# Performance work log

Hardware: AMD Instinct MI355X
Metric: run time of the kernel (lower is better)

## Reference

```python
import jax, jax.numpy as jnp
import numpy as np

BN_EPS = 1e-5

def _conv1x1(w, b, x):
    # w: (O, C), b: (O,), x: (B, C, T) -> (B, O, T)
    return jnp.einsum('oc,bct->bot', w, x) + b[None, :, None]

def _maxpool2(x):
    # MaxPool1d(kernel_size=2, stride=2): (B, C, T) -> (B, C, T//2)
    B, C, T = x.shape
    return x.reshape(B, C, T // 2, 2).max(axis=-1)

def setup_inputs() -> dict:
    key = jax.random.key(0)
    ks = jax.random.split(key, 11)
    B, C, Ci, T = 4, 256, 128, 8192
    s_in = 1.0 / np.sqrt(C)
    s_ic = 1.0 / np.sqrt(Ci)
    return {
        'x':       jax.random.normal(ks[0], (B, C, T), dtype=jnp.float32),
        'theta_w': jax.random.uniform(ks[1], (Ci, C), jnp.float32, -s_in, s_in),
        'theta_b': jax.random.uniform(ks[2], (Ci,),   jnp.float32, -s_in, s_in),
        'phi_w':   jax.random.uniform(ks[3], (Ci, C), jnp.float32, -s_in, s_in),
        'phi_b':   jax.random.uniform(ks[4], (Ci,),   jnp.float32, -s_in, s_in),
        'g_w':     jax.random.uniform(ks[5], (Ci, C), jnp.float32, -s_in, s_in),
        'g_b':     jax.random.uniform(ks[6], (Ci,),   jnp.float32, -s_in, s_in),
        'w_w':     jax.random.uniform(ks[7], (C, Ci), jnp.float32, -s_ic, s_ic),
        'w_b':     jax.random.uniform(ks[8], (C,),    jnp.float32, -s_ic, s_ic),
        'gamma':   jax.random.normal(ks[9], (C,), dtype=jnp.float32),
        'beta':    jax.random.normal(ks[10], (C,), dtype=jnp.float32),
    }

def reference(x, theta_w, theta_b, phi_w, phi_b, g_w, g_b, w_w, w_b, gamma, beta):
    # x: (B, C, T)
    theta = _conv1x1(theta_w, theta_b, x)            # (B, Ci, T)
    phi   = _maxpool2(_conv1x1(phi_w, phi_b, x))     # (B, Ci, N), N = T//2
    g     = _maxpool2(_conv1x1(g_w, g_b, x))         # (B, Ci, N)
    N = phi.shape[-1]
    # f = theta^T phi / N  (dot-product similarity, divide-by-N normalization)
    f = jnp.einsum('bct,bcn->btn', theta, phi) / N   # (B, T, N)
    y = jnp.einsum('btn,bcn->bct', f, g)             # (B, Ci, T)
    wy = _conv1x1(w_w, w_b, y)                       # (B, C, T)
    # BatchNorm1d (training mode: batch statistics over (B, T), biased var)
    mean = wy.mean(axis=(0, 2), keepdims=True)
    var = ((wy - mean) ** 2).mean(axis=(0, 2), keepdims=True)
    bn = gamma[None, :, None] * (wy - mean) * jax.lax.rsqrt(var + BN_EPS) + beta[None, :, None]
    return bn + x
```

## Files before the change

### kernel.cpp

```cpp
#include <hip/hip_runtime.h>
#include <hip/hip_bf16.h>


constexpr int B = 4, C = 256, CI = 128, T = 8192, NN = 4096;

using s16x8 = __attribute__((ext_vector_type(8))) short;
using f32x4 = __attribute__((ext_vector_type(4))) float;

__device__ __forceinline__ unsigned short f2bf(float f) {
    unsigned int x = __float_as_uint(f);
    unsigned int r = (x + 0x7fffu + ((x >> 16) & 1u)) >> 16;
    return (unsigned short)r;
}
__device__ __forceinline__ float bf2f(unsigned short u) {
    return __uint_as_float((unsigned int)u << 16);
}

#define MFMA(a, b, c) __builtin_amdgcn_mfma_f32_16x16x32_bf16((a), (b), (c), 0, 0, 0)

__device__ __forceinline__ void glds16(const unsigned short* g, void* l) {
    __builtin_amdgcn_global_load_lds(
        (const __attribute__((address_space(1))) unsigned int*)(g),
        (__attribute__((address_space(3))) unsigned int*)(l), 16, 0, 0);
}


constexpr size_t SZ_XT = (size_t)B * T * C * 2;
constexpr size_t O_XTH = 0;
constexpr size_t O_XTL = O_XTH + SZ_XT;
constexpr size_t O_WSH = O_XTL + SZ_XT;
constexpr size_t O_WSL = O_WSH + (size_t)C * C * 2;
constexpr size_t SZ_P  = (size_t)B * CI * NN * 2;
constexpr size_t O_PH  = O_WSL + (size_t)C * C * 2;
constexpr size_t O_PL  = O_PH + SZ_P;
constexpr size_t O_GH  = O_PL + SZ_P;
constexpr size_t O_GL  = O_GH + SZ_P;
constexpr size_t O_S   = O_GL + SZ_P;
constexpr size_t O_M   = O_S  + (size_t)B * CI * CI * 4;
constexpr size_t O_W2H = O_M  + (size_t)B * C * CI * 4;
constexpr size_t O_W2L = O_W2H + (size_t)B * C * C * 2;
constexpr size_t O_B2  = O_W2L + (size_t)B * C * C * 2;
constexpr size_t O_GS  = O_B2 + (size_t)B * C * 4;
constexpr size_t O_GQ  = O_GS + (size_t)C * 4;
constexpr size_t O_A   = O_GQ + (size_t)C * 4;
constexpr size_t O_SH  = O_A  + (size_t)C * 4;

__global__ __launch_bounds__(256) void k0_split(
    const float* __restrict__ x, unsigned short* __restrict__ xth,
    unsigned short* __restrict__ xtl)
{
    __shared__ float xs[64][65];
    int t0 = blockIdx.x * 64, c0 = blockIdx.y * 64, b = blockIdx.z;
    int tid = threadIdx.x;
    const float* xb = x + (size_t)b * C * T;
    #pragma unroll
    for (int p = 0; p < 4; ++p) {
        int idx = tid + p * 256;
        int cr = idx >> 4;
        int tg = (idx & 15) * 4;
        float4 v = *reinterpret_cast<const float4*>(xb + (size_t)(c0 + cr) * T + t0 + tg);
        xs[tg + 0][cr] = v.x; xs[tg + 1][cr] = v.y;
        xs[tg + 2][cr] = v.z; xs[tg + 3][cr] = v.w;
    }
    __syncthreads();
    size_t tileBase = ((size_t)b * (T / 128) + (t0 >> 7)) * 32768;
    int trBase = t0 & 127;
    #pragma unroll
    for (int p = 0; p < 2; ++p) {
        int idx = tid + p * 256;
        int kcL = idx >> 6;
        int tl  = idx & 63;
        s16x8 hs, ls;
        #pragma unroll
        for (int j = 0; j < 8; ++j) {
            float v = xs[tl][kcL * 8 + j];
            unsigned short h = f2bf(v);
            unsigned short l = f2bf(v - bf2f(h));
            hs[j] = (short)h; ls[j] = (short)l;
        }
        size_t dst = tileBase + (size_t)((c0 >> 3) + kcL) * 1024 + (trBase + tl) * 8;
        *reinterpret_cast<s16x8*>(xth + dst) = hs;
        *reinterpret_cast<s16x8*>(xtl + dst) = ls;
    }
}

__global__ __launch_bounds__(256) void k0w(
    const float* __restrict__ phi_w, const float* __restrict__ g_w,
    unsigned short* __restrict__ wsh, unsigned short* __restrict__ wsl)
{
    int idx = blockIdx.x * 256 + threadIdx.x;
    int c8 = idx & 31, row = idx >> 5;
    const float* src = (row < CI) ? &phi_w[(size_t)row * C + c8 * 8]
                                  : &g_w[(size_t)(row - CI) * C + c8 * 8];
    s16x8 hs, ls;
    #pragma unroll
    for (int j = 0; j < 8; ++j) {
        float v = src[j];
        unsigned short h = f2bf(v);
        hs[j] = (short)h; ls[j] = (short)f2bf(v - bf2f(h));
    }
    size_t dst = (size_t)(row >> 7) * 32768 + (size_t)c8 * 1024 + (row & 127) * 8;
    *reinterpret_cast<s16x8*>(wsh + dst) = hs;
    *reinterpret_cast<s16x8*>(wsl + dst) = ls;
}

#define STAGE_A(srcT) {                                                        \
    _Pragma("unroll")                                                          \
    for (int i_ = 0; i_ < 16; ++i_)                                            \
        glds16((srcT) + (size_t)(w * 8192 + i_ * 512 + lane * 8),              \
               arena + w * 16384 + i_ * 1024);                                 \
}

#define K8(BT) {                                                               \
    _Pragma("unroll")                                                          \
    for (int ks_ = 0; ks_ < 8; ++ks_) {                                        \
        s16x8 af[4], bfr[4];                                                   \
        _Pragma("unroll")                                                      \
        for (int ts_ = 0; ts_ < 4; ++ts_)                                      \
            af[ts_] = *(const s16x8*)(arena + (ks_ * 4 + lk) * 2048            \
                                      + (wt * 64 + ts_ * 16 + lr) * 16);       \
        _Pragma("unroll")                                                      \
        for (int os_ = 0; os_ < 4; ++os_)                                      \
            bfr[os_] = *(const s16x8*)((BT) + (size_t)(ks_ * 4 + lk) * 1024    \
                                       + (wo * 64 + os_ * 16 + lr) * 8);       \
        _Pragma("unroll")                                                      \
        for (int os_ = 0; os_ < 4; ++os_)                                      \
            _Pragma("unroll")                                                  \
            for (int ts_ = 0; ts_ < 4; ++ts_)                                  \
                acc[os_][ts_] = MFMA(af[ts_], bfr[os_], acc[os_][ts_]);        \
    }                                                                          \
}

#define GEMM_3PHASE(aT_h, aT_l, bT_h, bT_l) {                                  \
    STAGE_A(aT_h);                                                             \
    __syncthreads();                                                           \
    K8(bT_h);                                                                  \
    K8(bT_l);                                                                  \
    __syncthreads();                                                           \
    STAGE_A(aT_l);                                                             \
    __syncthreads();                                                           \
    K8(bT_h);                                                                  \
}

__global__ __launch_bounds__(256) void k1_mfma(
    const unsigned short* __restrict__ xth, const unsigned short* __restrict__ xtl,
    const unsigned short* __restrict__ wsh, const unsigned short* __restrict__ wsl,
    const float* __restrict__ phi_b, const float* __restrict__ g_b,
    unsigned short* __restrict__ ph, unsigned short* __restrict__ pl,
    unsigned short* __restrict__ gh, unsigned short* __restrict__ gl)
{
    const int b = blockIdx.z, t0 = blockIdx.x * 128, isG = blockIdx.y;
    __shared__ __align__(16) char arena[65536];
    const int tid = threadIdx.x, lane = tid & 63, w = tid >> 6;
    const int lr = lane & 15, lk = lane >> 4;
    const int wt = w >> 1, wo = w & 1;

    const unsigned short* aTh = xth + ((size_t)b * (T / 128) + (t0 >> 7)) * 32768;
    const unsigned short* aTl = xtl + ((size_t)b * (T / 128) + (t0 >> 7)) * 32768;
    const unsigned short* bTh = wsh + (size_t)isG * 32768;
    const unsigned short* bTl = wsl + (size_t)isG * 32768;

    f32x4 acc[4][4];
    #pragma unroll
    for (int i = 0; i < 4; ++i)
        #pragma unroll
        for (int j = 0; j < 4; ++j) acc[i][j] = (f32x4){0.f, 0.f, 0.f, 0.f};

    GEMM_3PHASE(aTh, aTl, bTh, bTl)
    __syncthreads();

    unsigned int (*pool_s)[65] = (unsigned int (*)[65])arena;
    const float* biasArr = isG ? g_b : phi_b;
    #pragma unroll
    for (int os = 0; os < 4; ++os) {
        int oL = wo * 64 + os * 16 + lr;
        float bias = biasArr[oL];
        #pragma unroll
        for (int ts = 0; ts < 4; ++ts) {
            f32x4 v = acc[os][ts];
            float m0 = fmaxf(v[0], v[1]) + bias;
            float m1 = fmaxf(v[2], v[3]) + bias;
            int nl = wt * 32 + ts * 8 + lk * 2;
            unsigned short h0 = f2bf(m0), h1 = f2bf(m1);
            pool_s[oL][nl]     = (unsigned int)h0 | ((unsigned int)f2bf(m0 - bf2f(h0)) << 16);
            pool_s[oL][nl + 1] = (unsigned int)h1 | ((unsigned int)f2bf(m1 - bf2f(h1)) << 16);
        }
    }
    __syncthreads();
    int oL = tid >> 1, seg = tid & 1;
    size_t n0 = (size_t)(t0 >> 1) + seg * 32;
    unsigned short* dh = (isG ? gh : ph) + ((size_t)b * CI + oL) * NN + n0;
    unsigned short* dl = (isG ? gl : pl) + ((size_t)b * CI + oL) * NN + n0;
    #pragma unroll
    for (int g4 = 0; g4 < 4; ++g4) {
        s16x8 hs, ls;
        #pragma unroll
        for (int j = 0; j < 8; ++j) {
            unsigned int u = pool_s[oL][seg * 32 + g4 * 8 + j];
            hs[j] = (short)(u & 0xffffu);
            ls[j] = (short)(u >> 16);
        }
        *reinterpret_cast<s16x8*>(dh + g4 * 8) = hs;
        *reinterpret_cast<s16x8*>(dl + g4 * 8) = ls;
    }
}

template <int MODE>
__global__ __launch_bounds__(256) void k45_mfma(
    const unsigned short* __restrict__ xth, const unsigned short* __restrict__ xtl,
    const unsigned short* __restrict__ w2h, const unsigned short* __restrict__ w2l,
    const float* __restrict__ b2, const float* __restrict__ x,
    const float* __restrict__ abuf, const float* __restrict__ shbuf,
    float* __restrict__ gsum, float* __restrict__ gsq, float* __restrict__ out)
{
    const int b = blockIdx.z, t0 = blockIdx.x * 128, oHalf = blockIdx.y;
    const int o0 = oHalf * 128;
    __shared__ __align__(16) char arena[65536];
    const int tid = threadIdx.x, lane = tid & 63, w = tid >> 6;
    const int lr = lane & 15, lk = lane >> 4;
    const int wt = w >> 1, wo = w & 1;

    const unsigned short* aTh = xth + ((size_t)b * (T / 128) + (t0 >> 7)) * 32768;
    const unsigned short* aTl = xtl + ((size_t)b * (T / 128) + (t0 >> 7)) * 32768;
    const unsigned short* bTh = w2h + ((size_t)b * 2 + oHalf) * 32768;
    const unsigned short* bTl = w2l + ((size_t)b * 2 + oHalf) * 32768;

    f32x4 acc[4][4];
    #pragma unroll
    for (int i = 0; i < 4; ++i)
        #pragma unroll
        for (int j = 0; j < 4; ++j) acc[i][j] = (f32x4){0.f, 0.f, 0.f, 0.f};

    GEMM_3PHASE(aTh, aTl, bTh, bTl)

    #pragma unroll
    for (int os = 0; os < 4; ++os) {
        int o = o0 + wo * 64 + os * 16 + lr;
        float bv = b2[(size_t)b * C + o];
        if (MODE == 0) {
            float s = 0.f, q = 0.f;
            #pragma unroll
            for (int ts = 0; ts < 4; ++ts)
                #pragma unroll
                for (int r = 0; r < 4; ++r) {
                    float v = acc[os][ts][r] + bv;
                    s += v; q += v * v;
                }
            s += __shfl_xor(s, 16); s += __shfl_xor(s, 32);
            q += __shfl_xor(q, 16); q += __shfl_xor(q, 32);
            if (lk == 0) { atomicAdd(&gsum[o], s); atomicAdd(&gsq[o], q); }
        } else {
            float av = abuf[o], sv = shbuf[o];
            #pragma unroll
            for (int ts = 0; ts < 4; ++ts) {
                int t = t0 + wt * 64 + ts * 16 + lk * 4;
                size_t base = ((size_t)b * C + o) * T + t;
                float4 xv = *reinterpret_cast<const float4*>(x + base);
                float4 ov;
                ov.x = av * (acc[os][ts][0] + bv) + sv + xv.x;
                ov.y = av * (acc[os][ts][1] + bv) + sv + xv.y;
                ov.z = av * (acc[os][ts][2] + bv) + sv + xv.z;
                ov.w = av * (acc[os][ts][3] + bv) + sv + xv.w;
                *reinterpret_cast<float4*>(out + base) = ov;
            }
        }
    }
}

__global__ __launch_bounds__(256) void k2_mfma(
    const unsigned short* __restrict__ ph, const unsigned short* __restrict__ pl,
    const unsigned short* __restrict__ gh, const unsigned short* __restrict__ gl,
    float* __restrict__ S)
{
    int b = blockIdx.y, n0 = blockIdx.x * 128;
    int tid = threadIdx.x, lane = tid & 63, w = tid >> 6;
    int lr = lane & 15, lk = lane >> 4;

    f32x4 acc[2][8];
    #pragma unroll
    for (int i = 0; i < 2; ++i)
        #pragma unroll
        for (int j = 0; j < 8; ++j) acc[i][j] = (f32x4){0.f, 0.f, 0.f, 0.f};

    const unsigned short* ah_b = gh + ((size_t)b * CI + w * 32 + lr) * NN + n0 + lk * 8;
    const unsigned short* al_b = gl + ((size_t)b * CI + w * 32 + lr) * NN + n0 + lk * 8;
    const unsigned short* bh_b = ph + ((size_t)b * CI + lr) * NN + n0 + lk * 8;
    const unsigned short* bl_b = pl + ((size_t)b * CI + lr) * NN + n0 + lk * 8;

    for (int ks = 0; ks < 4; ++ks) {
        s16x8 Ah[2], Al[2], Bh[8], Bl[8];
        #pragma unroll
        for (int is = 0; is < 2; ++is) {
            Ah[is] = *reinterpret_cast<const s16x8*>(ah_b + (size_t)is * 16 * NN + ks * 32);
            Al[is] = *reinterpret_cast<const s16x8*>(al_b + (size_t)is * 16 * NN + ks * 32);
        }
        #pragma unroll
        for (int js = 0; js < 8; ++js) {
            Bh[js] = *reinterpret_cast<const s16x8*>(bh_b + (size_t)js * 16 * NN + ks * 32);
            Bl[js] = *reinterpret_cast<const s16x8*>(bl_b + (size_t)js * 16 * NN + ks * 32);
        }
        #pragma unroll
        for (int is = 0; is < 2; ++is)
            #pragma unroll
            for (int js = 0; js < 8; ++js) {
                acc[is][js] = MFMA(Ah[is], Bh[js], acc[is][js]);
                acc[is][js] = MFMA(Al[is], Bh[js], acc[is][js]);
                acc[is][js] = MFMA(Ah[is], Bl[js], acc[is][js]);
            }
    }
    #pragma unroll
    for (int is = 0; is < 2; ++is) {
        int i0 = w * 32 + is * 16 + lk * 4;
        #pragma unroll
        for (int js = 0; js < 8; ++js) {
            int j = js * 16 + lr;
            #pragma unroll
            for (int r = 0; r < 4; ++r)
                atomicAdd(&S[((size_t)b * CI + i0 + r) * CI + j], acc[is][js][r]);
        }
    }
}

__global__ __launch_bounds__(256) void k3a_M(
    const float* __restrict__ w_w, const float* __restrict__ S, float* __restrict__ M)
{
    int idx = blockIdx.x * 256 + threadIdx.x;
    int j4 = (idx & 31) * 4;
    int r  = (idx >> 5) & (C - 1);
    int b  = idx >> 13;
    const float* Sb = S + (size_t)b * CI * CI;
    const float* wr = w_w + (size_t)r * CI;
    float4 a = {0.f, 0.f, 0.f, 0.f};
    for (int k = 0; k < CI; ++k) {
        float wv = wr[k];
        float4 s = *reinterpret_cast<const float4*>(&Sb[(size_t)k * CI + j4]);
        a.x += wv * s.x; a.y += wv * s.y; a.z += wv * s.z; a.w += wv * s.w;
    }
    const float sc = 1.f / NN;
    a.x *= sc; a.y *= sc; a.z *= sc; a.w *= sc;
    *reinterpret_cast<float4*>(&M[((size_t)b * C + r) * CI + j4]) = a;
}

__global__ __launch_bounds__(256) void k3b_W2(
    const float* __restrict__ M, const float* __restrict__ theta_w,
    const float* __restrict__ theta_b, const float* __restrict__ w_b,
    unsigned short* __restrict__ w2h, unsigned short* __restrict__ w2l,
    float* __restrict__ b2)
{
    int idx = blockIdx.x * 256 + threadIdx.x;
    int c8 = idx & 31;
    int r  = (idx >> 5) & (C - 1);
    int b  = idx >> 13;
    const float* Mb = M + ((size_t)b * C + r) * CI;
    float4 a0 = {0.f, 0.f, 0.f, 0.f}, a1 = {0.f, 0.f, 0.f, 0.f};
    for (int k = 0; k < CI; ++k) {
        float mv = Mb[k];
        const float* tw = &theta_w[(size_t)k * C + c8 * 8];
        float4 t0 = *reinterpret_cast<const float4*>(tw);
        float4 t1 = *reinterpret_cast<const float4*>(tw + 4);
        a0.x += mv * t0.x; a0.y += mv * t0.y; a0.z += mv * t0.z; a0.w += mv * t0.w;
        a1.x += mv * t1.x; a1.y += mv * t1.y; a1.z += mv * t1.z; a1.w += mv * t1.w;
    }
    float av[8] = {a0.x, a0.y, a0.z, a0.w, a1.x, a1.y, a1.z, a1.w};
    s16x8 hs, ls;
    #pragma unroll
    for (int i = 0; i < 8; ++i) {
        unsigned short h = f2bf(av[i]);
        hs[i] = (short)h; ls[i] = (short)f2bf(av[i] - bf2f(h));
    }
    size_t dst = ((size_t)b * 2 + (r >> 7)) * 32768 + (size_t)c8 * 1024 + (r & 127) * 8;
    *reinterpret_cast<s16x8*>(w2h + dst) = hs;
    *reinterpret_cast<s16x8*>(w2l + dst) = ls;
    if (c8 == 0) {
        float bv = 0.f;
        for (int k = 0; k < CI; ++k) bv += Mb[k] * theta_b[k];
        b2[(size_t)b * C + r] = bv + w_b[r];
    }
}

__global__ void k4b_stats(const float* __restrict__ gsum, const float* __restrict__ gsq,
                          const float* __restrict__ gamma, const float* __restrict__ beta,
                          float* __restrict__ a, float* __restrict__ sh)
{
    int c = threadIdx.x;
    const float invBT = 1.f / (float)(B * T);
    float mean = gsum[c] * invBT;
    float var  = gsq[c] * invBT - mean * mean;
    float av = gamma[c] * rsqrtf(var + 1e-5f);
    a[c]  = av;
    sh[c] = beta[c] - av * mean;
}

extern "C" void kernel_launch(void* const* d_in, const int* in_sizes, int n_in,
                              void* d_out, int out_size, void* d_ws, size_t ws_size,
                              hipStream_t stream)
{
    const float* x       = (const float*)d_in[0];
    const float* theta_w = (const float*)d_in[1];
    const float* theta_b = (const float*)d_in[2];
    const float* phi_w   = (const float*)d_in[3];
    const float* phi_b   = (const float*)d_in[4];
    const float* g_w     = (const float*)d_in[5];
    const float* g_b     = (const float*)d_in[6];
    const float* w_w     = (const float*)d_in[7];
    const float* w_b     = (const float*)d_in[8];
    const float* gamma   = (const float*)d_in[9];
    const float* beta    = (const float*)d_in[10];
    float* out = (float*)d_out;
    char* ws = (char*)d_ws;

    unsigned short* xth = (unsigned short*)(ws + O_XTH);
    unsigned short* xtl = (unsigned short*)(ws + O_XTL);
    unsigned short* wsh = (unsigned short*)(ws + O_WSH);
    unsigned short* wsl = (unsigned short*)(ws + O_WSL);
    unsigned short* ph  = (unsigned short*)(ws + O_PH);
    unsigned short* pl  = (unsigned short*)(ws + O_PL);
    unsigned short* gh  = (unsigned short*)(ws + O_GH);
    unsigned short* gl  = (unsigned short*)(ws + O_GL);
    float* Sbuf  = (float*)(ws + O_S);
    float* Mbuf  = (float*)(ws + O_M);
    unsigned short* w2h = (unsigned short*)(ws + O_W2H);
    unsigned short* w2l = (unsigned short*)(ws + O_W2L);
    float* b2    = (float*)(ws + O_B2);
    float* gsum  = (float*)(ws + O_GS);
    float* gsq   = (float*)(ws + O_GQ);
    float* abuf  = (float*)(ws + O_A);
    float* shbuf = (float*)(ws + O_SH);

    hipMemsetAsync(Sbuf, 0, (size_t)B * CI * CI * sizeof(float), stream);
    hipMemsetAsync(gsum, 0, 2 * (size_t)C * sizeof(float), stream);

    k0_split<<<dim3(T / 64, C / 64, B), 256, 0, stream>>>(x, xth, xtl);
    k0w<<<dim3(32), 256, 0, stream>>>(phi_w, g_w, wsh, wsl);
    k1_mfma<<<dim3(T / 128, 2, B), 256, 0, stream>>>(xth, xtl, wsh, wsl, phi_b, g_b,
                                                     ph, pl, gh, gl);
    k2_mfma<<<dim3(NN / 128, B), 256, 0, stream>>>(ph, pl, gh, gl, Sbuf);
    k3a_M<<<dim3(B * C * CI / 4 / 256), 256, 0, stream>>>(w_w, Sbuf, Mbuf);
    k3b_W2<<<dim3(B * C * C / 8 / 256), 256, 0, stream>>>(Mbuf, theta_w, theta_b, w_b,
                                                          w2h, w2l, b2);
    k45_mfma<0><<<dim3(T / 128, C / 128, B), 256, 0, stream>>>(
        xth, xtl, w2h, w2l, b2, x, abuf, shbuf, gsum, gsq, out);
    k4b_stats<<<1, C, 0, stream>>>(gsum, gsq, gamma, beta, abuf, shbuf);
    k45_mfma<1><<<dim3(T / 128, C / 128, B), 256, 0, stream>>>(
        xth, xtl, w2h, w2l, b2, x, abuf, shbuf, gsum, gsq, out);
}
```

Measured before the change: 253.4 us.

## Store bf16 conv output once and apply BatchNorm in a streaming pass

The first output GEMM pass now writes the pre-BN result as bf16 into scratch memory that reuses the phi buffer, while also accumulating the per-channel statistics. A new elementwise kernel then applies the BN scale, shift and residual, replacing the second full GEMM recomputation. Several MFMA kernels also get launch bounds requesting two blocks per CU. Rounding wy to bf16 reduces output precision and adds an extra write and read of the intermediate.

```diff
diff --git a/kernel.cpp b/kernel.cpp
--- a/kernel.cpp
+++ b/kernel.cpp
@@ -35,6 +35,7 @@
 constexpr size_t O_PL  = O_PH + SZ_P;
 constexpr size_t O_GH  = O_PL + SZ_P;
 constexpr size_t O_GL  = O_GH + SZ_P;
+constexpr size_t O_WY  = O_PH;
 constexpr size_t O_S   = O_GL + SZ_P;
 constexpr size_t O_M   = O_S  + (size_t)B * CI * CI * 4;
 constexpr size_t O_W2H = O_M  + (size_t)B * C * CI * 4;
@@ -142,7 +143,7 @@
     K8(bT_h);                                                                  \
 }
 
-__global__ __launch_bounds__(256) void k1_mfma(
+__global__ __launch_bounds__(256, 2) void k1_mfma(
     const unsigned short* __restrict__ xth, const unsigned short* __restrict__ xtl,
     const unsigned short* __restrict__ wsh, const unsigned short* __restrict__ wsl,
     const float* __restrict__ phi_b, const float* __restrict__ g_b,
@@ -205,13 +206,11 @@
     }
 }
 
-template <int MODE>
-__global__ __launch_bounds__(256) void k45_mfma(
+__global__ __launch_bounds__(256, 2) void k45_stats(
     const unsigned short* __restrict__ xth, const unsigned short* __restrict__ xtl,
     const unsigned short* __restrict__ w2h, const unsigned short* __restrict__ w2l,
-    const float* __restrict__ b2, const float* __restrict__ x,
-    const float* __restrict__ abuf, const float* __restrict__ shbuf,
-    float* __restrict__ gsum, float* __restrict__ gsq, float* __restrict__ out)
+    const float* __restrict__ b2, unsigned short* __restrict__ wy,
+    float* __restrict__ gsum, float* __restrict__ gsq)
 {
     const int b = blockIdx.z, t0 = blockIdx.x * 128, oHalf = blockIdx.y;
     const int o0 = oHalf * 128;
@@ -237,37 +236,62 @@
     for (int os = 0; os < 4; ++os) {
         int o = o0 + wo * 64 + os * 16 + lr;
         float bv = b2[(size_t)b * C + o];
-        if (MODE == 0) {
-            float s = 0.f, q = 0.f;
-            #pragma unroll
-            for (int ts = 0; ts < 4; ++ts)
-                #pragma unroll
-                for (int r = 0; r < 4; ++r) {
-                    float v = acc[os][ts][r] + bv;
-                    s += v; q += v * v;
-                }
-            s += __shfl_xor(s, 16); s += __shfl_xor(s, 32);
-            q += __shfl_xor(q, 16); q += __shfl_xor(q, 32);
-            if (lk == 0) { atomicAdd(&gsum[o], s); atomicAdd(&gsq[o], q); }
-        } else {
-            float av = abuf[o], sv = shbuf[o];
-            #pragma unroll
-            for (int ts = 0; ts < 4; ++ts) {
-                int t = t0 + wt * 64 + ts * 16 + lk * 4;
-                size_t base = ((size_t)b * C + o) * T + t;
-                float4 xv = *reinterpret_cast<const float4*>(x + base);
-                float4 ov;
-                ov.x = av * (acc[os][ts][0] + bv) + sv + xv.x;
-                ov.y = av * (acc[os][ts][1] + bv) + sv + xv.y;
-                ov.z = av * (acc[os][ts][2] + bv) + sv + xv.z;
-                ov.w = av * (acc[os][ts][3] + bv) + sv + xv.w;
-                *reinterpret_cast<float4*>(out + base) = ov;
-            }
-        }
-    }
-}
-
-__global__ __launch_bounds__(256) void k2_mfma(
+        float s = 0.f, q = 0.f;
+        #pragma unroll
+        for (int ts = 0; ts < 4; ++ts) {
+            int t = t0 + wt * 64 + ts * 16 + lk * 4;
+            ushort4 pk;
+            float v0 = acc[os][ts][0] + bv;
+            float v1 = acc[os][ts][1] + bv;
+            float v2 = acc[os][ts][2] + bv;
+            float v3 = acc[os][ts][3] + bv;
+            s += v0 + v1 + v2 + v3;
+            q += v0 * v0 + v1 * v1 + v2 * v2 + v3 * v3;
+            pk.x = f2bf(v0); pk.y = f2bf(v1); pk.z = f2bf(v2); pk.w = f2bf(v3);
+            *reinterpret_cast<ushort4*>(&wy[((size_t)b * C + o) * T + t]) = pk;
+        }
+        s += __shfl_xor(s, 16); s += __shfl_xor(s, 32);
+        q += __shfl_xor(q, 16); q += __shfl_xor(q, 32);
+        if (lk == 0) { atomicAdd(&gsum[o], s); atomicAdd(&gsq[o], q); }
+    }
+}
+
+__global__ void k4b_stats(const float* __restrict__ gsum, const float* __restrict__ gsq,
+                          const float* __restrict__ gamma, const float* __restrict__ beta,
+                          float* __restrict__ a, float* __restrict__ sh)
+{
+    int c = threadIdx.x;
+    const float invBT = 1.f / (float)(B * T);
+    float mean = gsum[c] * invBT;
+    float var  = gsq[c] * invBT - mean * mean;
+    float av = gamma[c] * rsqrtf(var + 1e-5f);
+    a[c]  = av;
+    sh[c] = beta[c] - av * mean;
+}
+
+__global__ __launch_bounds__(256) void k5_apply(
+    const float* __restrict__ x, const unsigned short* __restrict__ wy,
+    const float* __restrict__ a, const float* __restrict__ sh,
+    float* __restrict__ out)
+{
+    size_t total4 = (size_t)B * C * T / 4;
+    for (size_t i = (size_t)blockIdx.x * blockDim.x + threadIdx.x; i < total4;
+         i += (size_t)gridDim.x * blockDim.x) {
+        size_t e = i * 4;
+        int c = (int)((e / T) % C);
+        ushort4 w4 = *reinterpret_cast<const ushort4*>(&wy[e]);
+        float4 x4 = reinterpret_cast<const float4*>(x)[i];
+        float av = a[c], sv = sh[c];
+        float4 o;
+        o.x = av * bf2f(w4.x) + sv + x4.x;
+        o.y = av * bf2f(w4.y) + sv + x4.y;
+        o.z = av * bf2f(w4.z) + sv + x4.z;
+        o.w = av * bf2f(w4.w) + sv + x4.w;
+        reinterpret_cast<float4*>(out)[i] = o;
+    }
+}
+
+__global__ __launch_bounds__(256, 2) void k2_mfma(
     const unsigned short* __restrict__ ph, const unsigned short* __restrict__ pl,
     const unsigned short* __restrict__ gh, const unsigned short* __restrict__ gl,
     float* __restrict__ S)
@@ -378,19 +402,6 @@
     }
 }
 
-__global__ void k4b_stats(const float* __restrict__ gsum, const float* __restrict__ gsq,
-                          const float* __restrict__ gamma, const float* __restrict__ beta,
-                          float* __restrict__ a, float* __restrict__ sh)
-{
-    int c = threadIdx.x;
-    const float invBT = 1.f / (float)(B * T);
-    float mean = gsum[c] * invBT;
-    float var  = gsq[c] * invBT - mean * mean;
-    float av = gamma[c] * rsqrtf(var + 1e-5f);
-    a[c]  = av;
-    sh[c] = beta[c] - av * mean;
-}
-
 extern "C" void kernel_launch(void* const* d_in, const int* in_sizes, int n_in,
                               void* d_out, int out_size, void* d_ws, size_t ws_size,
                               hipStream_t stream)
@@ -417,6 +428,7 @@
     unsigned short* pl  = (unsigned short*)(ws + O_PL);
     unsigned short* gh  = (unsigned short*)(ws + O_GH);
     unsigned short* gl  = (unsigned short*)(ws + O_GL);
+    unsigned short* wy  = (unsigned short*)(ws + O_WY);
     float* Sbuf  = (float*)(ws + O_S);
     float* Mbuf  = (float*)(ws + O_M);
     unsigned short* w2h = (unsigned short*)(ws + O_W2H);
@@ -438,9 +450,8 @@
     k3a_M<<<dim3(B * C * CI / 4 / 256), 256, 0, stream>>>(w_w, Sbuf, Mbuf);
     k3b_W2<<<dim3(B * C * C / 8 / 256), 256, 0, stream>>>(Mbuf, theta_w, theta_b, w_b,
                                                           w2h, w2l, b2);
-    k45_mfma<0><<<dim3(T / 128, C / 128, B), 256, 0, stream>>>(
-        xth, xtl, w2h, w2l, b2, x, abuf, shbuf, gsum, gsq, out);
+    k45_stats<<<dim3(T / 128, C / 128, B), 256, 0, stream>>>(
+        xth, xtl, w2h, w2l, b2, wy, gsum, gsq);
     k4b_stats<<<1, C, 0, stream>>>(gsum, gsq, gamma, beta, abuf, shbuf);
-    k45_mfma<1><<<dim3(T / 128, C / 128, B), 256, 0, stream>>>(
-        xth, xtl, w2h, w2l, b2, x, abuf, shbuf, gsum, gsq, out);
-}
+    k5_apply<<<2048, 256, 0, stream>>>(x, wy, abuf, shbuf, out);
+}
```

Measured after the change: 243.6 us. 1.04x faster.
